# Optimization experiments

Hardware: AMD Instinct MI355X
Metric: run time of the kernel (lower is better)

## Reference

```python
import jax, jax.numpy as jnp
import numpy as np

N = 4096
D = 256
TEMP = 0.1
NEG_INF = -1e30
NUM_IDS = 1000
NUM_CAMS = 8


def setup_inputs() -> dict:
    key = jax.random.key(0)
    k1, k2, k3 = jax.random.split(key, 3)
    features = jax.random.normal(k1, (N, 2, D), dtype=jnp.float32)
    label = jax.random.randint(k2, (N,), 0, NUM_IDS)
    camid = jax.random.randint(k3, (N,), 0, NUM_CAMS)
    return {"features": features, "label": label, "camid": camid}


def reference(features, label, camid):
    n = features.shape[0]
    n2 = 2 * n
    # torch.cat(torch.unbind(features, dim=1), dim=0): [N,2,D] -> [2N,D]
    f = jnp.concatenate([features[:, 0], features[:, 1]], axis=0)
    # pairwise similarity, pre-scaled by 1/temperature (original divides each
    # per-positive logit row by T, which is equivalent)
    logit = jnp.matmul(f, f.T) / TEMP  # [2N, 2N]
    diag = jnp.eye(n2, dtype=bool)
    lg = jnp.where(diag, NEG_INF, logit)  # diagonal excluded by masked_select
    m = jnp.max(lg, axis=1, keepdims=True)  # stable shift per row
    e = jnp.exp(lg - m)  # exp(logit - m), 0 on diagonal

    label_eq = label[:, None] == label[None, :]          # [N, N]
    cam_eq = camid[:, None] == camid[None, :]
    pos_id = jnp.tile(label_eq, (2, 2))                  # label_mask.repeat(2,2)
    pos_cam = jnp.tile(label_eq & cam_eq, (2, 2))        # is_pos.repeat(2,2)

    def branch(pos_full, row_scale):
        pm = pos_full & ~diag        # positives (off-diagonal)
        nm = ~pos_full               # negatives (diagonal is positive -> excluded)
        neg_sum = jnp.sum(jnp.where(nm, e, 0.0), axis=1, keepdims=True)
        # per-positive CE with label 0 over [positive, negatives]:
        #   log(exp(l_p - m) + neg_sum) + m - l_p
        per = jnp.log(jnp.where(pm, e + neg_sum, 1.0)) - (lg - m)
        num_pos = jnp.sum(pm, axis=1).astype(lg.dtype)
        row = jnp.sum(jnp.where(pm, per, 0.0), axis=1) / num_pos
        return row_scale * row

    loss_rows = branch(pos_id, 1.0) + branch(pos_cam, 0.5)
    loss = jnp.sum(loss_rows) / n2
    return loss
```

## Files before the change

### kernel.cpp

```cpp
#include <hip/hip_runtime.h>

typedef __attribute__((ext_vector_type(8))) _Float16 h8v;
typedef __attribute__((ext_vector_type(4))) float    f4v;

#define N_   4096
#define N2   8192
#define D_   256
#define NIDS 1000
#define LCAP 32

constexpr float LN2F   = 0.6931471805599453f;
constexpr float NEGINF = -1e30f;
constexpr float SQRT_K = 3.7982826f;

__device__ __forceinline__ const float* frow(const float* f, int r) {
    return f + (size_t)(r & (N_ - 1)) * (2 * D_) + (size_t)((r >> 12) * D_);
}

__device__ __forceinline__ void gload_lds16(const void* g, void* l) {
    __builtin_amdgcn_global_load_lds(
        (const __attribute__((address_space(1))) void*)g,
        (__attribute__((address_space(3))) void*)l, 16, 0, 0);
}

__global__ __launch_bounds__(256) void prepK(const float* __restrict__ feat,
                                             const int* __restrict__ label,
                                             _Float16* __restrict__ f16,
                                             int* __restrict__ lists,
                                             int* __restrict__ idxmap,
                                             int* __restrict__ done) {
    if (blockIdx.x < 1024) {
        if (blockIdx.x == 0 && threadIdx.x == 0) *done = 0;
        int t = blockIdx.x * 256 + threadIdx.x;
        int r = t >> 5, g = t & 31;
        const float* src = frow(feat, r) + g * 8;
        float4 v0 = *(const float4*)src;
        float4 v1 = *(const float4*)(src + 4);
        float x[8] = {v0.x, v0.y, v0.z, v0.w, v1.x, v1.y, v1.z, v1.w};
        h8v h;
        #pragma unroll
        for (int i = 0; i < 8; ++i) h[i] = (_Float16)(x[i] * SQRT_K);
        *(h8v*)(f16 + (size_t)r * D_ + g * 8) = h;
    } else {
        int cls  = (blockIdx.x - 1024) * 4 + (threadIdx.x >> 6);
        int lane = threadIdx.x & 63;
        int* Lp = lists + (size_t)cls * (LCAP + 1);
        int cnt = 0;
        for (int jj = 0; jj < N_; jj += 64) {
            unsigned long long mk = __ballot(label[jj + lane] == cls);
            while (mk) {
                int b = __ffsll((unsigned long long)mk) - 1;
                mk &= mk - 1;
                if (lane == 0 && cnt < LCAP) {
                    Lp[1 + cnt] = jj + b;
                    idxmap[jj + b] = cnt;
                }
                ++cnt;
            }
        }
        if (lane == 0) Lp[0] = (cnt < LCAP) ? cnt : LCAP;
    }
}

__global__ __launch_bounds__(256, 4) void phaseA(const _Float16* __restrict__ f16,
                                                 const int* __restrict__ label,
                                                 const int* __restrict__ idxmap,
                                                 float2* __restrict__ partial,
                                                 float* __restrict__ plog) {
    __shared__ char lds[32768];

    const int tid  = threadIdx.x;
    const int lane = tid & 63;
    const int w    = tid >> 6;
    const int wr   = w >> 1, wc = w & 1;

    int idx = (blockIdx.x & 7) * 260 + (blockIdx.x >> 3);
    int rt = 0, rem = idx;
    while (rem >= 64 - rt) { rem -= 64 - rt; ++rt; }
    const int ct = rt + rem;
    const bool offdiag = (ct != rt);
    const int rowBase = rt * 128, colBase = ct * 128;

    f4v acc[4][4];
    #pragma unroll
    for (int i = 0; i < 4; ++i)
        #pragma unroll
        for (int j = 0; j < 4; ++j) acc[i][j] = (f4v){0.f, 0.f, 0.f, 0.f};

    const int prB = (w < 2) ? rowBase : colBase;
    const int ssrc = (lane & 3) ^ ((lane >> 3) & 3);
    const _Float16* gl = f16 + (size_t)(prB + (w & 1) * 64 + (lane >> 2)) * D_ + ssrc * 8;
    const int ldoff = ((w >= 2) ? 8192 : 0) + (w & 1) * 4096 + lane * 16;

    #pragma unroll
    for (int i = 0; i < 4; ++i)
        gload_lds16(gl + (size_t)i * 16 * D_, lds + ldoff + i * 1024);
    __syncthreads();

    const int l15  = lane & 15;
    const int phys = ((lane >> 4) ^ ((l15 >> 1) & 3)) * 16;
    const int aoff0 = (wr * 64 + l15) * 64 + phys;
    const int boff0 = 8192 + (wc * 64 + l15) * 64 + phys;

    for (int kc = 0; kc < 8; ++kc) {
        const int cur = kc & 1;
        if (kc < 7) {
            const _Float16* gk = gl + (kc + 1) * 32;
            char* lp = lds + (cur ^ 1) * 16384 + ldoff;
            #pragma unroll
            for (int i = 0; i < 4; ++i)
                gload_lds16(gk + (size_t)i * 16 * D_, lp + i * 1024);
        }
        const char* bb = lds + cur * 16384;
        h8v a[4], b[4];
        #pragma unroll
        for (int rf = 0; rf < 4; ++rf) a[rf] = *(const h8v*)(bb + aoff0 + rf * 1024);
        #pragma unroll
        for (int cf = 0; cf < 4; ++cf) b[cf] = *(const h8v*)(bb + boff0 + cf * 1024);
        #pragma unroll
        for (int rf = 0; rf < 4; ++rf)
            #pragma unroll
            for (int cf = 0; cf < 4; ++cf)
                acc[rf][cf] = __builtin_amdgcn_mfma_f32_16x16x32_f16(a[rf], b[cf], acc[rf][cf], 0, 0, 0);
        __syncthreads();
    }

    float* rowm    = (float*)lds;
    float* colm    = (float*)(lds + 16896);
    float* mrowS   = (float*)(lds + 21504);
    float* mcolS   = (float*)(lds + 22016);
    int*   rowIdxS = (int*)(lds + 22528);
    int*   colIdxS = (int*)(lds + 23040);

    if (tid < 128) {
        rowIdxS[tid] = idxmap[(rowBase + tid) & (N_ - 1)];
        colIdxS[tid] = idxmap[(colBase + tid) & (N_ - 1)];
    }

    const int grp32 = wc * 16 + l15;
    const int grp8  = wr * 4 + (lane >> 4);
    int rloc[16], cloc[4], rowlab[16], collab[4];
    #pragma unroll
    for (int rf = 0; rf < 4; ++rf)
        #pragma unroll
        for (int rg = 0; rg < 4; ++rg) {
            int i = rf * 4 + rg;
            rloc[i] = wr * 64 + rf * 16 + (lane >> 4) * 4 + rg;
            rowlab[i] = label[(rowBase + rloc[i]) & (N_ - 1)];
        }
    #pragma unroll
    for (int cf = 0; cf < 4; ++cf) {
        cloc[cf] = wc * 64 + cf * 16 + l15;
        collab[cf] = label[(colBase + cloc[cf]) & (N_ - 1)];
    }
    __syncthreads();

    #pragma unroll
    for (int rf = 0; rf < 4; ++rf)
        #pragma unroll
        for (int cf = 0; cf < 4; ++cf)
            #pragma unroll
            for (int rg = 0; rg < 4; ++rg) {
                int i = rf * 4 + rg;
                float v = acc[rf][cf][rg];
                bool match = (collab[cf] == rowlab[i]);
                if (match) {
                    int gr = rowBase + rloc[i], gc = colBase + cloc[cf];
                    if (gc > gr) {
                        plog[(size_t)gr * 64 + ((colIdxS[cloc[cf]] * 2 + (gc >> 12)) & 63)] = v;
                        plog[(size_t)gc * 64 + ((rowIdxS[rloc[i]] * 2 + (gr >> 12)) & 63)] = v;
                    }
                }
                acc[rf][cf][rg] = match ? NEGINF : v;
            }

    #pragma unroll
    for (int rf = 0; rf < 4; ++rf)
        #pragma unroll
        for (int rg = 0; rg < 4; ++rg) {
            float m = fmaxf(fmaxf(acc[rf][0][rg], acc[rf][1][rg]),
                            fmaxf(acc[rf][2][rg], acc[rf][3][rg]));
            rowm[rloc[rf * 4 + rg] * 33 + grp32] = m;
        }
    if (offdiag) {
        #pragma unroll
        for (int cf = 0; cf < 4; ++cf) {
            float m = NEGINF;
            #pragma unroll
            for (int rf = 0; rf < 4; ++rf)
                #pragma unroll
                for (int rg = 0; rg < 4; ++rg) m = fmaxf(m, acc[rf][cf][rg]);
            colm[cloc[cf] * 9 + grp8] = m;
        }
    }
    __syncthreads();
    if (tid < 128) {
        float m = NEGINF;
        #pragma unroll
        for (int g = 0; g < 32; ++g) m = fmaxf(m, rowm[tid * 33 + g]);
        mrowS[tid] = m;
        if (offdiag) {
            float mc = NEGINF;
            #pragma unroll
            for (int g = 0; g < 8; ++g) mc = fmaxf(mc, colm[tid * 9 + g]);
            mcolS[tid] = mc;
        }
    }
    __syncthreads();

    #pragma unroll
    for (int rf = 0; rf < 4; ++rf)
        #pragma unroll
        for (int rg = 0; rg < 4; ++rg) {
            int i = rf * 4 + rg;
            float m = mrowS[rloc[i]];
            float s = 0.f;
            #pragma unroll
            for (int cf = 0; cf < 4; ++cf) s += exp2f(acc[rf][cf][rg] - m);
            rowm[rloc[i] * 33 + grp32] = s;
        }
    if (offdiag) {
        #pragma unroll
        for (int cf = 0; cf < 4; ++cf) {
            float m = mcolS[cloc[cf]];
            float s = 0.f;
            #pragma unroll
            for (int rf = 0; rf < 4; ++rf)
                #pragma unroll
                for (int rg = 0; rg < 4; ++rg) s += exp2f(acc[rf][cf][rg] - m);
            colm[cloc[cf] * 9 + grp8] = s;
        }
    }
    __syncthreads();
    if (tid < 128) {
        float s = 0.f;
        #pragma unroll
        for (int g = 0; g < 32; ++g) s += rowm[tid * 33 + g];
        partial[(size_t)(rowBase + tid) * 64 + ct] = make_float2(mrowS[tid], s);
        if (offdiag) {
            float s2 = 0.f;
            #pragma unroll
            for (int g = 0; g < 8; ++g) s2 += colm[tid * 9 + g];
            partial[(size_t)(colBase + tid) * 64 + rt] = make_float2(mcolS[tid], s2);
        }
    }
}

__global__ __launch_bounds__(256) void phaseB(const int* __restrict__ label,
                                              const int* __restrict__ camid,
                                              const int* __restrict__ lists,
                                              const float2* __restrict__ partial,
                                              const float* __restrict__ plog,
                                              float* __restrict__ rowloss,
                                              int* __restrict__ done,
                                              float* __restrict__ out) {
    __shared__ float red[256];
    __shared__ int lastF;

    const int tid = threadIdx.x, lane = tid & 63, w = tid >> 6;
    const int row = blockIdx.x * 4 + w;
    const int rl = label[row & (N_ - 1)];
    const int rc = camid[row & (N_ - 1)];

    float2 p = partial[(size_t)row * 64 + lane];
    float mm = p.x, ms = p.y;
    #pragma unroll
    for (int off = 32; off >= 1; off >>= 1) {
        float om = __shfl_xor(mm, off), os = __shfl_xor(ms, off);
        float nm = fmaxf(mm, om);
        ms = ms * exp2f(mm - nm) + os * exp2f(om - nm);
        mm = nm;
    }
    const float cid = (mm + __log2f(ms)) * LN2F;

    const int* Lp = lists + (size_t)rl * (LCAP + 1);
    const int nmem = Lp[0];
    int member = (lane < 2 * nmem) ? Lp[1 + (lane >> 1)] : -1;
    int cand = member + (lane & 1) * N_;
    bool valid = (member >= 0) && (cand != row);
    float a_e = valid ? plog[(size_t)row * 64 + lane] * LN2F : NEGINF;
    int f_e = valid ? ((camid[member] == rc) ? 1 : 0) : 1;

    int cnt = __popcll(__ballot(valid));

    float xa = (valid && !f_e) ? a_e : NEGINF;
    float mx = xa;
    #pragma unroll
    for (int off = 32; off >= 1; off >>= 1) mx = fmaxf(mx, __shfl_xor(mx, off));
    float xe = (valid && !f_e) ? __expf(xa - mx) : 0.f;
    #pragma unroll
    for (int off = 32; off >= 1; off >>= 1) xe += __shfl_xor(xe, off);
    float ccam;
    if (xe > 0.f) {
        float xl = mx + __logf(xe);
        float d = xl - cid;
        ccam = (d <= 0.f) ? cid + log1pf(__expf(d)) : xl + log1pf(__expf(-d));
    } else {
        ccam = cid;
    }

    float ti = cid - a_e;
    float termid = (ti <= 0.f) ? log1pf(__expf(ti)) : ti + log1pf(__expf(-ti));
    termid = valid ? termid : 0.f;
    float tc = ccam - a_e;
    float termcam = (tc <= 0.f) ? log1pf(__expf(tc)) : tc + log1pf(__expf(-tc));
    termcam = (valid && f_e) ? termcam : 0.f;
    #pragma unroll
    for (int off = 32; off >= 1; off >>= 1) {
        termid  += __shfl_xor(termid, off);
        termcam += __shfl_xor(termcam, off);
    }
    int ncam = __popcll(__ballot(valid && f_e));
    if (lane == 0)
        rowloss[row] = termid / (float)cnt + 0.5f * termcam / (float)ncam;

    __syncthreads();
    if (tid == 0) {
        __threadfence();
        lastF = (atomicAdd(done, 1) == (int)gridDim.x - 1) ? 1 : 0;
    }
    __syncthreads();
    if (lastF) {
        __threadfence();
        float s = 0.f;
        const int b0 = tid * 32;
        #pragma unroll
        for (int i = 0; i < 32; ++i) s += rowloss[b0 + i];
        red[tid] = s;
        __syncthreads();
        for (int ww = 128; ww > 0; ww >>= 1) {
            if (tid < ww) red[tid] += red[tid + ww];
            __syncthreads();
        }
        if (tid == 0) out[0] = red[0] / (float)N2;
    }
}

extern "C" void kernel_launch(void* const* d_in, const int* in_sizes, int n_in,
                              void* d_out, int out_size, void* d_ws, size_t ws_size,
                              hipStream_t stream) {
    const float* feat  = (const float*)d_in[0];
    const int*   label = (const int*)d_in[1];
    const int*   camid = (const int*)d_in[2];

    _Float16* f16     = (_Float16*)d_ws;
    float2*   partial = (float2*)((char*)d_ws + 4u * 1024 * 1024);
    float*    plog    = (float*)((char*)d_ws + 8u * 1024 * 1024);
    float*    rowloss = (float*)((char*)d_ws + 10u * 1024 * 1024);
    int*      lists   = (int*)(rowloss + N2);
    int*      idxmap  = lists + NIDS * (LCAP + 1);
    int*      done    = idxmap + N_;

    prepK<<<1274, 256, 0, stream>>>(feat, label, f16, lists, idxmap, done);
    phaseA<<<2080, 256, 0, stream>>>(f16, label, idxmap, partial, plog);
    phaseB<<<2048, 256, 0, stream>>>(label, camid, lists, partial, plog,
                                     rowloss, done, (float*)d_out);
}
```

Baseline: 104.1 us.

## Fuse three kernels into one cooperative persistent kernel with grid syncs

Merges the prep, tile GEMM/softmax-partial, and per-row loss kernels into a single cooperative launch of 1024 blocks, separated by grid-wide barriers. The GEMM phase becomes a persistent loop that pulls tiles from an atomic counter, and each block handles two rows per wave in the final phase. The aim is to remove launch overhead and inter-kernel gaps. In exchange it adds grid-sync cost, requires all 1024 blocks to be co-resident (4 per CU), and may load-balance worse than the old 2080-block grid.

```diff
diff --git a/kernel.cpp b/kernel.cpp
--- a/kernel.cpp
+++ b/kernel.cpp
@@ -1,13 +1,18 @@
 #include <hip/hip_runtime.h>
+#include <hip/hip_cooperative_groups.h>
+
+namespace cg = cooperative_groups;
 
 typedef __attribute__((ext_vector_type(8))) _Float16 h8v;
 typedef __attribute__((ext_vector_type(4))) float    f4v;
 
-#define N_   4096
-#define N2   8192
-#define D_   256
-#define NIDS 1000
-#define LCAP 32
+#define N_     4096
+#define N2     8192
+#define D_     256
+#define NIDS   1000
+#define LCAP   32
+#define NTILES 2080
+#define GRID   1024
 
 constexpr float LN2F   = 0.6931471805599453f;
 constexpr float NEGINF = -1e30f;
@@ -23,15 +28,32 @@
         (__attribute__((address_space(3))) void*)l, 16, 0, 0);
 }
 
-__global__ __launch_bounds__(256) void prepK(const float* __restrict__ feat,
-                                             const int* __restrict__ label,
-                                             _Float16* __restrict__ f16,
-                                             int* __restrict__ lists,
-                                             int* __restrict__ idxmap,
-                                             int* __restrict__ done) {
-    if (blockIdx.x < 1024) {
-        if (blockIdx.x == 0 && threadIdx.x == 0) *done = 0;
-        int t = blockIdx.x * 256 + threadIdx.x;
+__global__ __launch_bounds__(256, 4) void mega(const float* __restrict__ feat,
+                                               const int* __restrict__ label,
+                                               const int* __restrict__ camid,
+                                               _Float16* __restrict__ f16,
+                                               float2* __restrict__ partial,
+                                               float* __restrict__ plog,
+                                               float* __restrict__ rowloss,
+                                               int* __restrict__ lists,
+                                               int* __restrict__ idxmap,
+                                               int* __restrict__ cnts,
+                                               float* __restrict__ out) {
+    cg::grid_group gg = cg::this_grid();
+
+    __shared__ char  lds[32768];
+    __shared__ int   sTile;
+    __shared__ float red[256];
+    __shared__ int   lastF;
+
+    const int bid  = blockIdx.x;
+    const int tid  = threadIdx.x;
+    const int lane = tid & 63;
+    const int w    = tid >> 6;
+
+    if (bid == 0 && tid == 0) { cnts[0] = 0; cnts[1] = 0; }
+    {
+        int t = bid * 256 + tid;
         int r = t >> 5, g = t & 31;
         const float* src = frow(feat, r) + g * 8;
         float4 v0 = *(const float4*)src;
@@ -41,9 +63,9 @@
         #pragma unroll
         for (int i = 0; i < 8; ++i) h[i] = (_Float16)(x[i] * SQRT_K);
         *(h8v*)(f16 + (size_t)r * D_ + g * 8) = h;
-    } else {
-        int cls  = (blockIdx.x - 1024) * 4 + (threadIdx.x >> 6);
-        int lane = threadIdx.x & 63;
+    }
+    if (bid < 250) {
+        int cls = bid * 4 + w;
         int* Lp = lists + (size_t)cls * (LCAP + 1);
         int cnt = 0;
         for (int jj = 0; jj < N_; jj += 64) {
@@ -60,264 +82,253 @@
         }
         if (lane == 0) Lp[0] = (cnt < LCAP) ? cnt : LCAP;
     }
-}
-
-__global__ __launch_bounds__(256, 4) void phaseA(const _Float16* __restrict__ f16,
-                                                 const int* __restrict__ label,
-                                                 const int* __restrict__ idxmap,
-                                                 float2* __restrict__ partial,
-                                                 float* __restrict__ plog) {
-    __shared__ char lds[32768];
-
-    const int tid  = threadIdx.x;
-    const int lane = tid & 63;
-    const int w    = tid >> 6;
-    const int wr   = w >> 1, wc = w & 1;
-
-    int idx = (blockIdx.x & 7) * 260 + (blockIdx.x >> 3);
-    int rt = 0, rem = idx;
-    while (rem >= 64 - rt) { rem -= 64 - rt; ++rt; }
-    const int ct = rt + rem;
-    const bool offdiag = (ct != rt);
-    const int rowBase = rt * 128, colBase = ct * 128;
-
-    f4v acc[4][4];
-    #pragma unroll
-    for (int i = 0; i < 4; ++i)
-        #pragma unroll
-        for (int j = 0; j < 4; ++j) acc[i][j] = (f4v){0.f, 0.f, 0.f, 0.f};
-
-    const int prB = (w < 2) ? rowBase : colBase;
-    const int ssrc = (lane & 3) ^ ((lane >> 3) & 3);
-    const _Float16* gl = f16 + (size_t)(prB + (w & 1) * 64 + (lane >> 2)) * D_ + ssrc * 8;
-    const int ldoff = ((w >= 2) ? 8192 : 0) + (w & 1) * 4096 + lane * 16;
-
-    #pragma unroll
-    for (int i = 0; i < 4; ++i)
-        gload_lds16(gl + (size_t)i * 16 * D_, lds + ldoff + i * 1024);
-    __syncthreads();
-
-    const int l15  = lane & 15;
-    const int phys = ((lane >> 4) ^ ((l15 >> 1) & 3)) * 16;
-    const int aoff0 = (wr * 64 + l15) * 64 + phys;
-    const int boff0 = 8192 + (wc * 64 + l15) * 64 + phys;
-
-    for (int kc = 0; kc < 8; ++kc) {
-        const int cur = kc & 1;
-        if (kc < 7) {
-            const _Float16* gk = gl + (kc + 1) * 32;
-            char* lp = lds + (cur ^ 1) * 16384 + ldoff;
-            #pragma unroll
-            for (int i = 0; i < 4; ++i)
-                gload_lds16(gk + (size_t)i * 16 * D_, lp + i * 1024);
-        }
-        const char* bb = lds + cur * 16384;
-        h8v a[4], b[4];
-        #pragma unroll
-        for (int rf = 0; rf < 4; ++rf) a[rf] = *(const h8v*)(bb + aoff0 + rf * 1024);
-        #pragma unroll
-        for (int cf = 0; cf < 4; ++cf) b[cf] = *(const h8v*)(bb + boff0 + cf * 1024);
+    gg.sync();
+
+    const int wr = w >> 1, wc = w & 1;
+    const int l15 = lane & 15;
+
+    for (;;) {
+        __syncthreads();
+        if (tid == 0) sTile = atomicAdd(&cnts[0], 1);
+        __syncthreads();
+        const int tk = sTile;
+        if (tk >= NTILES) break;
+
+        int idx = (tk & 7) * 260 + (tk >> 3);
+        int rt = 0, rem = idx;
+        while (rem >= 64 - rt) { rem -= 64 - rt; ++rt; }
+        const int ct = rt + rem;
+        const bool offdiag = (ct != rt);
+        const int rowBase = rt * 128, colBase = ct * 128;
+
+        f4v acc[4][4];
+        #pragma unroll
+        for (int i = 0; i < 4; ++i)
+            #pragma unroll
+            for (int j = 0; j < 4; ++j) acc[i][j] = (f4v){0.f, 0.f, 0.f, 0.f};
+
+        const int prB = (w < 2) ? rowBase : colBase;
+        const int ssrc = (lane & 3) ^ ((lane >> 3) & 3);
+        const _Float16* gl = f16 + (size_t)(prB + (w & 1) * 64 + (lane >> 2)) * D_ + ssrc * 8;
+        const int ldoff = ((w >= 2) ? 8192 : 0) + (w & 1) * 4096 + lane * 16;
+
+        #pragma unroll
+        for (int i = 0; i < 4; ++i)
+            gload_lds16(gl + (size_t)i * 16 * D_, lds + ldoff + i * 1024);
+        __syncthreads();
+
+        const int phys = ((lane >> 4) ^ ((l15 >> 1) & 3)) * 16;
+        const int aoff0 = (wr * 64 + l15) * 64 + phys;
+        const int boff0 = 8192 + (wc * 64 + l15) * 64 + phys;
+
+        for (int kc = 0; kc < 8; ++kc) {
+            const int cur = kc & 1;
+            if (kc < 7) {
+                const _Float16* gk = gl + (kc + 1) * 32;
+                char* lp = lds + (cur ^ 1) * 16384 + ldoff;
+                #pragma unroll
+                for (int i = 0; i < 4; ++i)
+                    gload_lds16(gk + (size_t)i * 16 * D_, lp + i * 1024);
+            }
+            const char* bb = lds + cur * 16384;
+            h8v a[4], b[4];
+            #pragma unroll
+            for (int rf = 0; rf < 4; ++rf) a[rf] = *(const h8v*)(bb + aoff0 + rf * 1024);
+            #pragma unroll
+            for (int cf = 0; cf < 4; ++cf) b[cf] = *(const h8v*)(bb + boff0 + cf * 1024);
+            #pragma unroll
+            for (int rf = 0; rf < 4; ++rf)
+                #pragma unroll
+                for (int cf = 0; cf < 4; ++cf)
+                    acc[rf][cf] = __builtin_amdgcn_mfma_f32_16x16x32_f16(a[rf], b[cf], acc[rf][cf], 0, 0, 0);
+            __syncthreads();
+        }
+
+        float* rowm    = (float*)lds;
+        float* colm    = (float*)(lds + 16896);
+        float* mrowS   = (float*)(lds + 21504);
+        float* mcolS   = (float*)(lds + 22016);
+        int*   rowIdxS = (int*)(lds + 22528);
+        int*   colIdxS = (int*)(lds + 23040);
+
+        if (tid < 128) {
+            rowIdxS[tid] = idxmap[(rowBase + tid) & (N_ - 1)];
+            colIdxS[tid] = idxmap[(colBase + tid) & (N_ - 1)];
+        }
+
+        const int grp32 = wc * 16 + l15;
+        const int grp8  = wr * 4 + (lane >> 4);
+        int rloc[16], cloc[4], rowlab[16], collab[4];
         #pragma unroll
         for (int rf = 0; rf < 4; ++rf)
-            #pragma unroll
-            for (int cf = 0; cf < 4; ++cf)
-                acc[rf][cf] = __builtin_amdgcn_mfma_f32_16x16x32_f16(a[rf], b[cf], acc[rf][cf], 0, 0, 0);
-        __syncthreads();
-    }
-
-    float* rowm    = (float*)lds;
-    float* colm    = (float*)(lds + 16896);
-    float* mrowS   = (float*)(lds + 21504);
-    float* mcolS   = (float*)(lds + 22016);
-    int*   rowIdxS = (int*)(lds + 22528);
-    int*   colIdxS = (int*)(lds + 23040);
-
-    if (tid < 128) {
-        rowIdxS[tid] = idxmap[(rowBase + tid) & (N_ - 1)];
-        colIdxS[tid] = idxmap[(colBase + tid) & (N_ - 1)];
-    }
-
-    const int grp32 = wc * 16 + l15;
-    const int grp8  = wr * 4 + (lane >> 4);
-    int rloc[16], cloc[4], rowlab[16], collab[4];
-    #pragma unroll
-    for (int rf = 0; rf < 4; ++rf)
-        #pragma unroll
-        for (int rg = 0; rg < 4; ++rg) {
-            int i = rf * 4 + rg;
-            rloc[i] = wr * 64 + rf * 16 + (lane >> 4) * 4 + rg;
-            rowlab[i] = label[(rowBase + rloc[i]) & (N_ - 1)];
-        }
-    #pragma unroll
-    for (int cf = 0; cf < 4; ++cf) {
-        cloc[cf] = wc * 64 + cf * 16 + l15;
-        collab[cf] = label[(colBase + cloc[cf]) & (N_ - 1)];
-    }
-    __syncthreads();
-
-    #pragma unroll
-    for (int rf = 0; rf < 4; ++rf)
-        #pragma unroll
-        for (int cf = 0; cf < 4; ++cf)
             #pragma unroll
             for (int rg = 0; rg < 4; ++rg) {
                 int i = rf * 4 + rg;
-                float v = acc[rf][cf][rg];
-                bool match = (collab[cf] == rowlab[i]);
-                if (match) {
-                    int gr = rowBase + rloc[i], gc = colBase + cloc[cf];
-                    if (gc > gr) {
-                        plog[(size_t)gr * 64 + ((colIdxS[cloc[cf]] * 2 + (gc >> 12)) & 63)] = v;
-                        plog[(size_t)gc * 64 + ((rowIdxS[rloc[i]] * 2 + (gr >> 12)) & 63)] = v;
+                rloc[i] = wr * 64 + rf * 16 + (lane >> 4) * 4 + rg;
+                rowlab[i] = label[(rowBase + rloc[i]) & (N_ - 1)];
+            }
+        #pragma unroll
+        for (int cf = 0; cf < 4; ++cf) {
+            cloc[cf] = wc * 64 + cf * 16 + l15;
+            collab[cf] = label[(colBase + cloc[cf]) & (N_ - 1)];
+        }
+        __syncthreads();
+
+        #pragma unroll
+        for (int rf = 0; rf < 4; ++rf)
+            #pragma unroll
+            for (int cf = 0; cf < 4; ++cf)
+                #pragma unroll
+                for (int rg = 0; rg < 4; ++rg) {
+                    int i = rf * 4 + rg;
+                    float v = acc[rf][cf][rg];
+                    bool match = (collab[cf] == rowlab[i]);
+                    if (match) {
+                        int gr = rowBase + rloc[i], gc = colBase + cloc[cf];
+                        if (gc > gr) {
+                            plog[(size_t)gr * 64 + ((colIdxS[cloc[cf]] * 2 + (gc >> 12)) & 63)] = v;
+                            plog[(size_t)gc * 64 + ((rowIdxS[rloc[i]] * 2 + (gr >> 12)) & 63)] = v;
+                        }
                     }
+                    acc[rf][cf][rg] = match ? NEGINF : v;
                 }
-                acc[rf][cf][rg] = match ? NEGINF : v;
-            }
-
-    #pragma unroll
-    for (int rf = 0; rf < 4; ++rf)
-        #pragma unroll
-        for (int rg = 0; rg < 4; ++rg) {
-            float m = fmaxf(fmaxf(acc[rf][0][rg], acc[rf][1][rg]),
-                            fmaxf(acc[rf][2][rg], acc[rf][3][rg]));
-            rowm[rloc[rf * 4 + rg] * 33 + grp32] = m;
-        }
-    if (offdiag) {
-        #pragma unroll
-        for (int cf = 0; cf < 4; ++cf) {
+
+        #pragma unroll
+        for (int rf = 0; rf < 4; ++rf)
+            #pragma unroll
+            for (int rg = 0; rg < 4; ++rg) {
+                float m = fmaxf(fmaxf(acc[rf][0][rg], acc[rf][1][rg]),
+                                fmaxf(acc[rf][2][rg], acc[rf][3][rg]));
+                rowm[rloc[rf * 4 + rg] * 33 + grp32] = m;
+            }
+        if (offdiag) {
+            #pragma unroll
+            for (int cf = 0; cf < 4; ++cf) {
+                float m = NEGINF;
+                #pragma unroll
+                for (int rf = 0; rf < 4; ++rf)
+                    #pragma unroll
+                    for (int rg = 0; rg < 4; ++rg) m = fmaxf(m, acc[rf][cf][rg]);
+                colm[cloc[cf] * 9 + grp8] = m;
+            }
+        }
+        __syncthreads();
+        if (tid < 128) {
             float m = NEGINF;
             #pragma unroll
-            for (int rf = 0; rf < 4; ++rf)
-                #pragma unroll
-                for (int rg = 0; rg < 4; ++rg) m = fmaxf(m, acc[rf][cf][rg]);
-            colm[cloc[cf] * 9 + grp8] = m;
-        }
-    }
-    __syncthreads();
-    if (tid < 128) {
-        float m = NEGINF;
-        #pragma unroll
-        for (int g = 0; g < 32; ++g) m = fmaxf(m, rowm[tid * 33 + g]);
-        mrowS[tid] = m;
+            for (int g = 0; g < 32; ++g) m = fmaxf(m, rowm[tid * 33 + g]);
+            mrowS[tid] = m;
+            if (offdiag) {
+                float mc = NEGINF;
+                #pragma unroll
+                for (int g = 0; g < 8; ++g) mc = fmaxf(mc, colm[tid * 9 + g]);
+                mcolS[tid] = mc;
+            }
+        }
+        __syncthreads();
+
+        #pragma unroll
+        for (int rf = 0; rf < 4; ++rf)
+            #pragma unroll
+            for (int rg = 0; rg < 4; ++rg) {
+                int i = rf * 4 + rg;
+                float m = mrowS[rloc[i]];
+                float s = 0.f;
+                #pragma unroll
+                for (int cf = 0; cf < 4; ++cf) s += exp2f(acc[rf][cf][rg] - m);
+                rowm[rloc[i] * 33 + grp32] = s;
+            }
         if (offdiag) {
-            float mc = NEGINF;
-            #pragma unroll
-            for (int g = 0; g < 8; ++g) mc = fmaxf(mc, colm[tid * 9 + g]);
-            mcolS[tid] = mc;
-        }
-    }
-    __syncthreads();
-
-    #pragma unroll
-    for (int rf = 0; rf < 4; ++rf)
-        #pragma unroll
-        for (int rg = 0; rg < 4; ++rg) {
-            int i = rf * 4 + rg;
-            float m = mrowS[rloc[i]];
+            #pragma unroll
+            for (int cf = 0; cf < 4; ++cf) {
+                float m = mcolS[cloc[cf]];
+                float s = 0.f;
+                #pragma unroll
+                for (int rf = 0; rf < 4; ++rf)
+                    #pragma unroll
+                    for (int rg = 0; rg < 4; ++rg) s += exp2f(acc[rf][cf][rg] - m);
+                colm[cloc[cf] * 9 + grp8] = s;
+            }
+        }
+        __syncthreads();
+        if (tid < 128) {
             float s = 0.f;
             #pragma unroll
-            for (int cf = 0; cf < 4; ++cf) s += exp2f(acc[rf][cf][rg] - m);
-            rowm[rloc[i] * 33 + grp32] = s;
-        }
-    if (offdiag) {
-        #pragma unroll
-        for (int cf = 0; cf < 4; ++cf) {
-            float m = mcolS[cloc[cf]];
-            float s = 0.f;
-            #pragma unroll
-            for (int rf = 0; rf < 4; ++rf)
-                #pragma unroll
-                for (int rg = 0; rg < 4; ++rg) s += exp2f(acc[rf][cf][rg] - m);
-            colm[cloc[cf] * 9 + grp8] = s;
-        }
-    }
-    __syncthreads();
-    if (tid < 128) {
-        float s = 0.f;
-        #pragma unroll
-        for (int g = 0; g < 32; ++g) s += rowm[tid * 33 + g];
-        partial[(size_t)(rowBase + tid) * 64 + ct] = make_float2(mrowS[tid], s);
-        if (offdiag) {
-            float s2 = 0.f;
-            #pragma unroll
-            for (int g = 0; g < 8; ++g) s2 += colm[tid * 9 + g];
-            partial[(size_t)(colBase + tid) * 64 + rt] = make_float2(mcolS[tid], s2);
-        }
-    }
-}
-
-__global__ __launch_bounds__(256) void phaseB(const int* __restrict__ label,
-                                              const int* __restrict__ camid,
-                                              const int* __restrict__ lists,
-                                              const float2* __restrict__ partial,
-                                              const float* __restrict__ plog,
-                                              float* __restrict__ rowloss,
-                                              int* __restrict__ done,
-                                              float* __restrict__ out) {
-    __shared__ float red[256];
-    __shared__ int lastF;
-
-    const int tid = threadIdx.x, lane = tid & 63, w = tid >> 6;
-    const int row = blockIdx.x * 4 + w;
-    const int rl = label[row & (N_ - 1)];
-    const int rc = camid[row & (N_ - 1)];
-
-    float2 p = partial[(size_t)row * 64 + lane];
-    float mm = p.x, ms = p.y;
-    #pragma unroll
-    for (int off = 32; off >= 1; off >>= 1) {
-        float om = __shfl_xor(mm, off), os = __shfl_xor(ms, off);
-        float nm = fmaxf(mm, om);
-        ms = ms * exp2f(mm - nm) + os * exp2f(om - nm);
-        mm = nm;
-    }
-    const float cid = (mm + __log2f(ms)) * LN2F;
-
-    const int* Lp = lists + (size_t)rl * (LCAP + 1);
-    const int nmem = Lp[0];
-    int member = (lane < 2 * nmem) ? Lp[1 + (lane >> 1)] : -1;
-    int cand = member + (lane & 1) * N_;
-    bool valid = (member >= 0) && (cand != row);
-    float a_e = valid ? plog[(size_t)row * 64 + lane] * LN2F : NEGINF;
-    int f_e = valid ? ((camid[member] == rc) ? 1 : 0) : 1;
-
-    int cnt = __popcll(__ballot(valid));
-
-    float xa = (valid && !f_e) ? a_e : NEGINF;
-    float mx = xa;
-    #pragma unroll
-    for (int off = 32; off >= 1; off >>= 1) mx = fmaxf(mx, __shfl_xor(mx, off));
-    float xe = (valid && !f_e) ? __expf(xa - mx) : 0.f;
-    #pragma unroll
-    for (int off = 32; off >= 1; off >>= 1) xe += __shfl_xor(xe, off);
-    float ccam;
-    if (xe > 0.f) {
-        float xl = mx + __logf(xe);
-        float d = xl - cid;
-        ccam = (d <= 0.f) ? cid + log1pf(__expf(d)) : xl + log1pf(__expf(-d));
-    } else {
-        ccam = cid;
-    }
-
-    float ti = cid - a_e;
-    float termid = (ti <= 0.f) ? log1pf(__expf(ti)) : ti + log1pf(__expf(-ti));
-    termid = valid ? termid : 0.f;
-    float tc = ccam - a_e;
-    float termcam = (tc <= 0.f) ? log1pf(__expf(tc)) : tc + log1pf(__expf(-tc));
-    termcam = (valid && f_e) ? termcam : 0.f;
-    #pragma unroll
-    for (int off = 32; off >= 1; off >>= 1) {
-        termid  += __shfl_xor(termid, off);
-        termcam += __shfl_xor(termcam, off);
-    }
-    int ncam = __popcll(__ballot(valid && f_e));
-    if (lane == 0)
-        rowloss[row] = termid / (float)cnt + 0.5f * termcam / (float)ncam;
+            for (int g = 0; g < 32; ++g) s += rowm[tid * 33 + g];
+            partial[(size_t)(rowBase + tid) * 64 + ct] = make_float2(mrowS[tid], s);
+            if (offdiag) {
+                float s2 = 0.f;
+                #pragma unroll
+                for (int g = 0; g < 8; ++g) s2 += colm[tid * 9 + g];
+                partial[(size_t)(colBase + tid) * 64 + rt] = make_float2(mcolS[tid], s2);
+            }
+        }
+    }
+    gg.sync();
+
+    #pragma unroll 1
+    for (int q = 0; q < 2; ++q) {
+        const int row = bid * 8 + w * 2 + q;
+        const int rl = label[row & (N_ - 1)];
+        const int rc = camid[row & (N_ - 1)];
+
+        float2 p = partial[(size_t)row * 64 + lane];
+        float mm = p.x, ms = p.y;
+        #pragma unroll
+        for (int off = 32; off >= 1; off >>= 1) {
+            float om = __shfl_xor(mm, off), os = __shfl_xor(ms, off);
+            float nm = fmaxf(mm, om);
+            ms = ms * exp2f(mm - nm) + os * exp2f(om - nm);
+            mm = nm;
+        }
+        const float cid = (mm + __log2f(ms)) * LN2F;
+
+        const int* Lp = lists + (size_t)rl * (LCAP + 1);
+        const int nmem = Lp[0];
+        int member = (lane < 2 * nmem) ? Lp[1 + (lane >> 1)] : -1;
+        int cand = member + (lane & 1) * N_;
+        bool valid = (member >= 0) && (cand != row);
+        float a_e = valid ? plog[(size_t)row * 64 + lane] * LN2F : NEGINF;
+        int f_e = valid ? ((camid[member] == rc) ? 1 : 0) : 1;
+
+        int cnt = __popcll(__ballot(valid));
+
+        float xa = (valid && !f_e) ? a_e : NEGINF;
+        float mx = xa;
+        #pragma unroll
+        for (int off = 32; off >= 1; off >>= 1) mx = fmaxf(mx, __shfl_xor(mx, off));
+        float xe = (valid && !f_e) ? __expf(xa - mx) : 0.f;
+        #pragma unroll
+        for (int off = 32; off >= 1; off >>= 1) xe += __shfl_xor(xe, off);
+        float ccam;
+        if (xe > 0.f) {
+            float xl = mx + __logf(xe);
+            float d = xl - cid;
+            ccam = (d <= 0.f) ? cid + log1pf(__expf(d)) : xl + log1pf(__expf(-d));
+        } else {
+            ccam = cid;
+        }
+
+        float ti = cid - a_e;
+        float termid = (ti <= 0.f) ? log1pf(__expf(ti)) : ti + log1pf(__expf(-ti));
+        termid = valid ? termid : 0.f;
+        float tc = ccam - a_e;
+        float termcam = (tc <= 0.f) ? log1pf(__expf(tc)) : tc + log1pf(__expf(-tc));
+        termcam = (valid && f_e) ? termcam : 0.f;
+        #pragma unroll
+        for (int off = 32; off >= 1; off >>= 1) {
+            termid  += __shfl_xor(termid, off);
+            termcam += __shfl_xor(termcam, off);
+        }
+        int ncam = __popcll(__ballot(valid && f_e));
+        if (lane == 0)
+            rowloss[row] = termid / (float)cnt + 0.5f * termcam / (float)ncam;
+    }
 
     __syncthreads();
     if (tid == 0) {
         __threadfence();
-        lastF = (atomicAdd(done, 1) == (int)gridDim.x - 1) ? 1 : 0;
+        lastF = (atomicAdd(&cnts[1], 1) == GRID - 1) ? 1 : 0;
     }
     __syncthreads();
     if (lastF) {
@@ -349,10 +360,12 @@
     float*    rowloss = (float*)((char*)d_ws + 10u * 1024 * 1024);
     int*      lists   = (int*)(rowloss + N2);
     int*      idxmap  = lists + NIDS * (LCAP + 1);
-    int*      done    = idxmap + N_;
-
-    prepK<<<1274, 256, 0, stream>>>(feat, label, f16, lists, idxmap, done);
-    phaseA<<<2080, 256, 0, stream>>>(f16, label, idxmap, partial, plog);
-    phaseB<<<2048, 256, 0, stream>>>(label, camid, lists, partial, plog,
-                                     rowloss, done, (float*)d_out);
+    int*      cnts    = idxmap + N_;
+    float*    outp    = (float*)d_out;
+
+    void* kargs[] = {(void*)&feat, (void*)&label, (void*)&camid, (void*)&f16,
+                     (void*)&partial, (void*)&plog, (void*)&rowloss,
+                     (void*)&lists, (void*)&idxmap, (void*)&cnts, (void*)&outp};
+    hipLaunchCooperativeKernel((const void*)mega, dim3(GRID), dim3(256),
+                               kargs, 0, stream);
 }
```

Result: slower. 328.7 us (+215.7%).
